# Performance work log

Measured on AMD Instinct MI355X. Metric: run time of the kernel, lower is better.

The kernel has to match this reference:

```python
import jax, jax.numpy as jnp
import numpy as np

B, D, P, E, C = 2048, 4096, 64, 8, 64
K = D // P  # conv kernel = stride = input_dim / patch_num


def setup_inputs() -> dict:
    key = jax.random.key(0)
    k1, k2, k3, k4 = jax.random.split(key, 4)
    x = jax.random.normal(k1, (B, 1, D), jnp.float32)
    router_w = jax.random.normal(k2, (E, K), jnp.float32) * 0.02   # Router conv weight [E,1,K] squeezed
    expert_w = jax.random.normal(k3, (E, 2 * C, K), jnp.float32) * 0.001  # per-expert conv weights (small=True scaling)
    expert_b = jax.random.normal(k4, (E, 2 * C), jnp.float32) * 0.001
    return {"x": x, "router_w": router_w, "expert_w": expert_w, "expert_b": expert_b}


def reference(x, router_w, expert_w, expert_b):
    b, _, d = x.shape
    e, k = router_w.shape
    p = d // k
    c = expert_w.shape[1] // 2

    # Conv1d(1, ch, K, stride=K) == per-patch matmul; sum over dim 2 == sum over patches.
    patches = x.reshape(b, p, k)                                   # [B,P,K]

    # Router (eval mode: no noise)
    select = jnp.einsum('bpk,ek->be', patches, router_w)           # [B,E]

    # top1 routing
    gate = jnp.max(select, axis=-1)                                # [B]
    index = jnp.argmax(select, axis=-1)                            # [B]
    onehot = jax.nn.one_hot(index, e, dtype=select.dtype)          # [B,E]

    # aux load-balance loss
    density = onehot.mean(axis=0)
    density_proxy = select.mean(axis=0)
    loss = (density_proxy * density).mean() * float(e ** 2)

    # combine/dispatch (mask_flat is all ones for top1)
    combine = gate[:, None] * onehot                               # [B,E]
    dispatch = jax.lax.stop_gradient((combine != 0).astype(select.dtype))  # bool cast detaches grad
    select0 = dispatch

    # Dense dispatch: every expert sees the full batch, zero-masked by dispatch.
    # z[e,b,c,p] = conv of (dispatch[b,e]*x[b]) with expert e's kernel, + bias
    z = jnp.einsum('bpk,eck->ebcp', patches, expert_w)             # [E,B,2C,P]
    z = z * dispatch.T[:, :, None, None] + expert_b[:, None, :, None]
    z = z ** 3                                                     # nonlinear=True
    s = z.sum(axis=-1)                                             # sum over patches -> [E,B,2C]
    expert_out = jnp.stack([s[..., :c].sum(-1), s[..., c:].sum(-1)], axis=-1)  # [E,B,2]

    out = jnp.einsum('be,ebl->bl', combine, expert_out)            # [B,2]
    out = jax.nn.softmax(out, axis=1)
    return out, select0, loss
```

## Files before the change

kernel.cpp:

```cpp
#include <hip/hip_runtime.h>

#define BB 2048
#define DD 4096
#define PP 64
#define KK 64
#define EE 8
#define C2 128
#define NBLK BB

typedef __attribute__((ext_vector_type(8))) short short8;
typedef __attribute__((ext_vector_type(4))) float floatx4;

__device__ inline unsigned pack2_trunc(float lo, float hi) {
    unsigned ul = __builtin_bit_cast(unsigned, lo);
    unsigned uh = __builtin_bit_cast(unsigned, hi);
    return (uh & 0xFFFF0000u) | (ul >> 16);
}

__device__ inline void gload16(const float* src, float* lds_dst_uniform) {
    __builtin_amdgcn_global_load_lds(
        (const __attribute__((address_space(1))) unsigned int*)src,
        (__attribute__((address_space(3))) unsigned int*)lds_dst_uniform, 16, 0, 0);
}

__global__ __launch_bounds__(256) void moe_main(
    const float* __restrict__ x, const float* __restrict__ rw,
    const float* __restrict__ ew, const float* __restrict__ eb,
    float* __restrict__ out, float* __restrict__ ws)
{
    __shared__ float xs[64 * 64];
    __shared__ float sh_h[4];
    const int lane = threadIdx.x & 63;
    const int w = threadIdx.x >> 6;
    const int b = blockIdx.x;
    const int r = lane & 15, q = lane >> 4;
    const float* xb = x + (size_t)b * DD;

    #pragma unroll
    for (int j = 0; j < 4; ++j) {
        const int row = (w * 4 + j) * 4 + (lane >> 4);
        const int g   = (lane & 15) ^ (row & 7);
        gload16(xb + row * 64 + g * 4, &xs[(w * 4 + j) * 256]);
    }
    __syncthreads();

    const int s = r & 7;
    float ps[16];
    #pragma unroll
    for (int j = 0; j < 16; ++j) ps[j] = 0.f;
    short8 af[8];
    #pragma unroll
    for (int mt = 0; mt < 4; ++mt) {
        #pragma unroll
        for (int kb = 0; kb < 2; ++kb) {
            const float* base = &xs[(mt * 16 + r) * 64 + kb * 32];
            float4 v0 = *(const float4*)(base + (((q * 2 + 0) ^ s) << 2));
            float4 v1 = *(const float4*)(base + (((q * 2 + 1) ^ s) << 2));
            ps[kb*8+0] += v0.x; ps[kb*8+1] += v0.y; ps[kb*8+2] += v0.z; ps[kb*8+3] += v0.w;
            ps[kb*8+4] += v1.x; ps[kb*8+5] += v1.y; ps[kb*8+6] += v1.z; ps[kb*8+7] += v1.w;
            uint4 u;
            u.x = pack2_trunc(v0.x, v0.y); u.y = pack2_trunc(v0.z, v0.w);
            u.z = pack2_trunc(v1.x, v1.y); u.w = pack2_trunc(v1.z, v1.w);
            af[mt * 2 + kb] = __builtin_bit_cast(short8, u);
        }
    }

    float d[8];
    #pragma unroll
    for (int e2 = 0; e2 < 8; ++e2) {
        const float* rwe = rw + e2 * KK;
        float4 a0 = *(const float4*)(rwe + q * 8);
        float4 a1 = *(const float4*)(rwe + q * 8 + 4);
        float4 b0 = *(const float4*)(rwe + 32 + q * 8);
        float4 b1 = *(const float4*)(rwe + 32 + q * 8 + 4);
        float t = ps[0]*a0.x + ps[1]*a0.y + ps[2]*a0.z + ps[3]*a0.w
                + ps[4]*a1.x + ps[5]*a1.y + ps[6]*a1.z + ps[7]*a1.w
                + ps[8]*b0.x + ps[9]*b0.y + ps[10]*b0.z + ps[11]*b0.w
                + ps[12]*b1.x + ps[13]*b1.y + ps[14]*b1.z + ps[15]*b1.w;
        t += __shfl_xor(t, 1);  t += __shfl_xor(t, 2);  t += __shfl_xor(t, 4);
        t += __shfl_xor(t, 8);  t += __shfl_xor(t, 16); t += __shfl_xor(t, 32);
        d[e2] = t;
    }
    float gate = d[0]; int e = 0;
    #pragma unroll
    for (int e2 = 1; e2 < 8; ++e2)
        if (d[e2] > gate) { gate = d[e2]; e = e2; }

    if (w == 0 && lane < 8) {
        float on = (gate != 0.f) ? 1.f : 0.f;
        out[BB * 2 + b * 8 + lane] = (lane == e) ? on : 0.f;
        ws[b * 16 + lane]     = d[lane];
        ws[b * 16 + 8 + lane] = (lane == e) ? 1.f : 0.f;
    }

    const float* we = ew + (size_t)e * (C2 * KK);
    float h = 0.f;
    #pragma unroll
    for (int ntl = 0; ntl < 2; ++ntl) {
        const int nt = w * 2 + ntl;
        float bs = eb[e * C2 + nt * 16 + r];
        const float* wr = we + (nt * 16 + r) * KK + q * 8;
        float4 w0 = *(const float4*)wr;
        float4 w1 = *(const float4*)(wr + 4);
        float4 w2 = *(const float4*)(wr + 32);
        float4 w3 = *(const float4*)(wr + 36);
        uint4 u0, u1;
        u0.x = pack2_trunc(w0.x, w0.y); u0.y = pack2_trunc(w0.z, w0.w);
        u0.z = pack2_trunc(w1.x, w1.y); u0.w = pack2_trunc(w1.z, w1.w);
        u1.x = pack2_trunc(w2.x, w2.y); u1.y = pack2_trunc(w2.z, w2.w);
        u1.z = pack2_trunc(w3.x, w3.y); u1.w = pack2_trunc(w3.z, w3.w);
        short8 bf0 = __builtin_bit_cast(short8, u0);
        short8 bf1 = __builtin_bit_cast(short8, u1);
        #pragma unroll
        for (int mt = 0; mt < 4; ++mt) {
            floatx4 a4 = (floatx4){0.f, 0.f, 0.f, 0.f};
            a4 = __builtin_amdgcn_mfma_f32_16x16x32_bf16(af[mt*2+0], bf0, a4, 0, 0, 0);
            a4 = __builtin_amdgcn_mfma_f32_16x16x32_bf16(af[mt*2+1], bf1, a4, 0, 0, 0);
            #pragma unroll
            for (int i = 0; i < 4; ++i) {
                float z = a4[i] + bs;
                h = fmaf(z * z, z, h);
            }
        }
    }
    #pragma unroll
    for (int off = 1; off < 64; off <<= 1)
        h += __shfl_xor(h, off);

    if (lane == 0) sh_h[w] = h;
    __syncthreads();

    if (threadIdx.x == 0) {
        float l0 = gate * (sh_h[0] + sh_h[1]);
        float l1 = gate * (sh_h[2] + sh_h[3]);
        float m = fmaxf(l0, l1);
        float e0 = __expf(l0 - m), e1 = __expf(l1 - m);
        float inv = 1.f / (e0 + e1);
        float2 o; o.x = e0 * inv; o.y = e1 * inv;
        *(float2*)(out + b * 2) = o;
    }
}

__global__ __launch_bounds__(256) void loss2(
    const float* __restrict__ ws, float* __restrict__ out)
{
    __shared__ float red[4][16];
    const int t = threadIdx.x;
    const int w = t >> 6, lane = t & 63;

    float p[8] = {0,0,0,0,0,0,0,0};
    float c[8] = {0,0,0,0,0,0,0,0};
    #pragma unroll
    for (int it = 0; it < BB / 256; ++it) {
        const float4* row = (const float4*)(ws + (size_t)(it * 256 + t) * 16);
        float4 r0 = row[0], r1 = row[1], r2 = row[2], r3 = row[3];
        p[0] += r0.x; p[1] += r0.y; p[2] += r0.z; p[3] += r0.w;
        p[4] += r1.x; p[5] += r1.y; p[6] += r1.z; p[7] += r1.w;
        c[0] += r2.x; c[1] += r2.y; c[2] += r2.z; c[3] += r2.w;
        c[4] += r3.x; c[5] += r3.y; c[6] += r3.z; c[7] += r3.w;
    }
    #pragma unroll
    for (int off = 32; off > 0; off >>= 1) {
        #pragma unroll
        for (int e2 = 0; e2 < 8; ++e2) {
            p[e2] += __shfl_xor(p[e2], off);
            c[e2] += __shfl_xor(c[e2], off);
        }
    }
    if (lane == 0) {
        #pragma unroll
        for (int e2 = 0; e2 < 8; ++e2) { red[w][e2] = p[e2]; red[w][8 + e2] = c[e2]; }
    }
    __syncthreads();
    if (t == 0) {
        float loss = 0.f;
        #pragma unroll
        for (int e2 = 0; e2 < 8; ++e2) {
            float sp = red[0][e2] + red[1][e2] + red[2][e2] + red[3][e2];
            float sc = red[0][8 + e2] + red[1][8 + e2] + red[2][8 + e2] + red[3][8 + e2];
            loss += (sp * (1.f / BB)) * (sc * (1.f / BB));
        }
        out[BB * 2 + BB * 8] = loss * (float)EE;
    }
}

extern "C" void kernel_launch(void* const* d_in, const int* in_sizes, int n_in,
                              void* d_out, int out_size, void* d_ws, size_t ws_size,
                              hipStream_t stream) {
    (void)in_sizes; (void)n_in; (void)out_size; (void)ws_size;
    const float* x  = (const float*)d_in[0];
    const float* rw = (const float*)d_in[1];
    const float* ew = (const float*)d_in[2];
    const float* eb = (const float*)d_in[3];
    float* out = (float*)d_out;
    float* ws  = (float*)d_ws;

    moe_main<<<NBLK, 256, 0, stream>>>(x, rw, ew, eb, out, ws);
    loss2<<<1, 256, 0, stream>>>(ws, out);
}
```

Before: 98.84 us.

## Fuse loss reduction into main kernel via atomics and last-block finalize

Removes the separate single-block loss kernel. Each block atomically accumulates its router logits and expert counts into global accumulators, and the last block to finish (tracked by an atomic counter) computes the loss and resets the accumulators. This saves a kernel launch and the workspace round trip. In exchange it adds contention from 2048 blocks doing atomics on 16 addresses, and makes the summation order nondeterministic.

```diff
diff --git a/kernel.cpp b/kernel.cpp
--- a/kernel.cpp
+++ b/kernel.cpp
@@ -10,6 +10,9 @@
 
 typedef __attribute__((ext_vector_type(8))) short short8;
 typedef __attribute__((ext_vector_type(4))) float floatx4;
+
+__device__ unsigned g_ctr = 0u;
+__device__ float g_acc[16] = {};
 
 __device__ inline unsigned pack2_trunc(float lo, float hi) {
     unsigned ul = __builtin_bit_cast(unsigned, lo);
@@ -26,7 +29,7 @@
 __global__ __launch_bounds__(256) void moe_main(
     const float* __restrict__ x, const float* __restrict__ rw,
     const float* __restrict__ ew, const float* __restrict__ eb,
-    float* __restrict__ out, float* __restrict__ ws)
+    float* __restrict__ out)
 {
     __shared__ float xs[64 * 64];
     __shared__ float sh_h[4];
@@ -89,8 +92,8 @@
     if (w == 0 && lane < 8) {
         float on = (gate != 0.f) ? 1.f : 0.f;
         out[BB * 2 + b * 8 + lane] = (lane == e) ? on : 0.f;
-        ws[b * 16 + lane]     = d[lane];
-        ws[b * 16 + 8 + lane] = (lane == e) ? 1.f : 0.f;
+        atomicAdd(&g_acc[lane], d[lane]);
+        if (lane == e) atomicAdd(&g_acc[8 + lane], 1.f);
     }
 
     const float* we = ew + (size_t)e * (C2 * KK);
@@ -129,7 +132,6 @@
 
     if (lane == 0) sh_h[w] = h;
     __syncthreads();
-
     if (threadIdx.x == 0) {
         float l0 = gate * (sh_h[0] + sh_h[1]);
         float l1 = gate * (sh_h[2] + sh_h[3]);
@@ -138,63 +140,36 @@
         float inv = 1.f / (e0 + e1);
         float2 o; o.x = e0 * inv; o.y = e1 * inv;
         *(float2*)(out + b * 2) = o;
-    }
-}
 
-__global__ __launch_bounds__(256) void loss2(
-    const float* __restrict__ ws, float* __restrict__ out)
-{
-    __shared__ float red[4][16];
-    const int t = threadIdx.x;
-    const int w = t >> 6, lane = t & 63;
-
-    float p[8] = {0,0,0,0,0,0,0,0};
-    float c[8] = {0,0,0,0,0,0,0,0};
-    #pragma unroll
-    for (int it = 0; it < BB / 256; ++it) {
-        const float4* row = (const float4*)(ws + (size_t)(it * 256 + t) * 16);
-        float4 r0 = row[0], r1 = row[1], r2 = row[2], r3 = row[3];
-        p[0] += r0.x; p[1] += r0.y; p[2] += r0.z; p[3] += r0.w;
-        p[4] += r1.x; p[5] += r1.y; p[6] += r1.z; p[7] += r1.w;
-        c[0] += r2.x; c[1] += r2.y; c[2] += r2.z; c[3] += r2.w;
-        c[4] += r3.x; c[5] += r3.y; c[6] += r3.z; c[7] += r3.w;
-    }
-    #pragma unroll
-    for (int off = 32; off > 0; off >>= 1) {
-        #pragma unroll
-        for (int e2 = 0; e2 < 8; ++e2) {
-            p[e2] += __shfl_xor(p[e2], off);
-            c[e2] += __shfl_xor(c[e2], off);
+        __threadfence();
+        unsigned old = __hip_atomic_fetch_add(&g_ctr, 1u,
+                                              __ATOMIC_ACQ_REL, __HIP_MEMORY_SCOPE_AGENT);
+        if ((old & (NBLK - 1u)) == NBLK - 1u) {
+            float loss = 0.f;
+            #pragma unroll
+            for (int e2 = 0; e2 < 8; ++e2) {
+                float sp = __hip_atomic_load(&g_acc[e2],     __ATOMIC_RELAXED, __HIP_MEMORY_SCOPE_AGENT);
+                float sc = __hip_atomic_load(&g_acc[8 + e2], __ATOMIC_RELAXED, __HIP_MEMORY_SCOPE_AGENT);
+                loss += (sp * (1.f / BB)) * (sc * (1.f / BB));
+            }
+            out[BB * 2 + BB * 8] = loss * (float)EE;
+            #pragma unroll
+            for (int i = 0; i < 16; ++i)
+                __hip_atomic_store(&g_acc[i], 0.f,
+                                   __ATOMIC_RELAXED, __HIP_MEMORY_SCOPE_AGENT);
         }
-    }
-    if (lane == 0) {
-        #pragma unroll
-        for (int e2 = 0; e2 < 8; ++e2) { red[w][e2] = p[e2]; red[w][8 + e2] = c[e2]; }
-    }
-    __syncthreads();
-    if (t == 0) {
-        float loss = 0.f;
-        #pragma unroll
-        for (int e2 = 0; e2 < 8; ++e2) {
-            float sp = red[0][e2] + red[1][e2] + red[2][e2] + red[3][e2];
-            float sc = red[0][8 + e2] + red[1][8 + e2] + red[2][8 + e2] + red[3][8 + e2];
-            loss += (sp * (1.f / BB)) * (sc * (1.f / BB));
-        }
-        out[BB * 2 + BB * 8] = loss * (float)EE;
     }
 }
 
 extern "C" void kernel_launch(void* const* d_in, const int* in_sizes, int n_in,
                               void* d_out, int out_size, void* d_ws, size_t ws_size,
                               hipStream_t stream) {
-    (void)in_sizes; (void)n_in; (void)out_size; (void)ws_size;
+    (void)in_sizes; (void)n_in; (void)out_size; (void)d_ws; (void)ws_size;
     const float* x  = (const float*)d_in[0];
     const float* rw = (const float*)d_in[1];
     const float* ew = (const float*)d_in[2];
     const float* eb = (const float*)d_in[3];
     float* out = (float*)d_out;
-    float* ws  = (float*)d_ws;
 
-    moe_main<<<NBLK, 256, 0, stream>>>(x, rw, ew, eb, out, ws);
-    loss2<<<1, 256, 0, stream>>>(ws, out);
+    moe_main<<<NBLK, 256, 0, stream>>>(x, rw, ew, eb, out);
 }
```

New measurement: 208.0 us. 110% more time.
